# Performance work log

Hardware: AMD Instinct MI355X
Metric: run time of the kernel (lower is better)

Reference implementation:

```python
import jax, jax.numpy as jnp
import numpy as np

CODEBOOK_SIZE = 32768
EMBED_DIM = 4


def setup_inputs() -> dict:
    key = jax.random.key(0)
    k1, k2 = jax.random.split(key)
    # [batch, temporal, channels, height, width]
    hidden_state = jax.random.normal(k1, (1, 4, EMBED_DIM, 48, 48), dtype=jnp.float32)
    # nn.Embedding weight, init uniform(-1/cb, 1/cb) as in the torch module
    embedding = jax.random.uniform(
        k2, (CODEBOOK_SIZE, EMBED_DIM), dtype=jnp.float32,
        minval=-1.0 / CODEBOOK_SIZE, maxval=1.0 / CODEBOOK_SIZE,
    )
    return {"hidden_state": hidden_state, "embedding": embedding}


def reference(hidden_state, embedding):
    b, t, c, h, w = hidden_state.shape
    # permute channels last, flatten to [N, C]
    x = jnp.transpose(hidden_state, (0, 1, 3, 4, 2)).reshape(-1, c)
    distances = (
        jnp.sum(x * x, axis=1, keepdims=True)
        + jnp.sum(embedding * embedding, axis=1)
        - 2.0 * jnp.einsum("nd,kd->nk", x, embedding)
    )
    min_encoding_indices = jnp.argmin(distances, axis=1)
    return min_encoding_indices.reshape(b, t, h, w)
```

## Files before the change

kernel.cpp:

```cpp
#include <hip/hip_runtime.h>
#include <cfloat>


#define ROWS  12
#define BLOCK 512
#define WAVES (BLOCK / 64)
#define NK    32768
#define EPT   2
#define CHUNK (BLOCK * EPT)

__device__ __forceinline__ float rlf(float v) {
    return __builtin_bit_cast(float,
        __builtin_amdgcn_readfirstlane(__builtin_bit_cast(int, v)));
}

__global__ __launch_bounds__(BLOCK)
__attribute__((amdgpu_waves_per_eu(3, 4)))
void vq_argmin_kernel(const float* __restrict__ hs,
                      const float4* __restrict__ cb,
                      int* __restrict__ out)
{
    __shared__ float sRD[WAVES * ROWS];
    __shared__ int   sRI[WAVES * ROWS];

    const int tid = threadIdx.x;
    const int rowbase = blockIdx.x * ROWS;

    float sx0[ROWS], sx1[ROWS], sx2[ROWS], sx3[ROWS], sq[ROWS];
    float best[ROWS];
    int   bidx[ROWS];

    #pragma unroll
    for (int r = 0; r < ROWS; ++r) {
        int n = rowbase + r;
        int t = n / 2304;
        int rem = n - t * 2304;
        const float* ptr = hs + t * 9216 + rem;
        float a0 = ptr[0], a1 = ptr[2304], a2 = ptr[4608], a3 = ptr[6912];
        float q = __fadd_rn(__fadd_rn(__fadd_rn(__fmul_rn(a0, a0),
                                                __fmul_rn(a1, a1)),
                                      __fmul_rn(a2, a2)),
                            __fmul_rn(a3, a3));
        sx0[r] = rlf(a0); sx1[r] = rlf(a1);
        sx2[r] = rlf(a2); sx3[r] = rlf(a3);
        sq[r]  = rlf(q);
        best[r] = FLT_MAX; bidx[r] = 0;
    }

    float4 bufA[EPT], bufB[EPT];

    auto load_chunk = [&](float4* buf, int tb) {
        #pragma unroll
        for (int j = 0; j < EPT; ++j) buf[j] = cb[tb + tid + j * BLOCK];
    };
    auto compute_chunk = [&](const float4* buf, int tb) {
        #pragma unroll
        for (int j = 0; j < EPT; ++j) {
            float4 e = buf[j];
            float e2 = __fadd_rn(__fadd_rn(__fadd_rn(__fmul_rn(e.x, e.x),
                                                     __fmul_rn(e.y, e.y)),
                                           __fmul_rn(e.z, e.z)),
                                 __fmul_rn(e.w, e.w));
            int m = tb / BLOCK + j;
            #pragma unroll
            for (int r = 0; r < ROWS; ++r) {
                float dot = __fmul_rn(sx0[r], e.x);
                dot = __fmaf_rn(sx1[r], e.y, dot);
                dot = __fmaf_rn(sx2[r], e.z, dot);
                dot = __fmaf_rn(sx3[r], e.w, dot);
                float t1 = __fadd_rn(sq[r], e2);
                float d  = __fmaf_rn(dot, -2.0f, t1);
                if (d < best[r]) { best[r] = d; bidx[r] = m; }
            }
        }
    };

    load_chunk(bufA, 0);
    for (int tb = 0; tb < NK; tb += 2 * CHUNK) {
        load_chunk(bufB, tb + CHUNK);
        compute_chunk(bufA, tb);
        int nb = tb + 2 * CHUNK < NK ? tb + 2 * CHUNK : 0;
        load_chunk(bufA, nb);
        compute_chunk(bufB, tb + CHUNK);
    }

    int kk[ROWS];
    #pragma unroll
    for (int r = 0; r < ROWS; ++r) kk[r] = bidx[r] * BLOCK + tid;

    #pragma unroll
    for (int r = 0; r < ROWS; ++r) {
        float d = best[r]; int i = kk[r];
        #pragma unroll
        for (int off = 32; off >= 1; off >>= 1) {
            float d2 = __shfl_xor(d, off, 64);
            int   i2 = __shfl_xor(i, off, 64);
            if (d2 < d || (d2 == d && i2 < i)) { d = d2; i = i2; }
        }
        best[r] = d; kk[r] = i;
    }

    int wave = tid >> 6;
    if ((tid & 63) == 0) {
        #pragma unroll
        for (int r = 0; r < ROWS; ++r) {
            sRD[wave * ROWS + r] = best[r];
            sRI[wave * ROWS + r] = kk[r];
        }
    }
    __syncthreads();

    if (tid < ROWS) {
        float d = sRD[tid]; int i = sRI[tid];
        #pragma unroll
        for (int w = 1; w < WAVES; ++w) {
            float d2 = sRD[w * ROWS + tid];
            int   i2 = sRI[w * ROWS + tid];
            if (d2 < d || (d2 == d && i2 < i)) { d = d2; i = i2; }
        }
        out[rowbase + tid] = i;
    }
}

extern "C" void kernel_launch(void* const* d_in, const int* in_sizes, int n_in,
                              void* d_out, int out_size, void* d_ws, size_t ws_size,
                              hipStream_t stream)
{
    const float*  hs = (const float*)d_in[0];
    const float4* cb = (const float4*)d_in[1];
    int* out = (int*)d_out;

    const int nrows = 9216;
    dim3 grid(nrows / ROWS), block(BLOCK);
    vq_argmin_kernel<<<grid, block, 0, stream>>>(hs, cb, out);
}
```

Baseline: 121.8 us.

## Split codebook across blocks with per-row atomicMin on packed distance-index keys

```diff
diff --git a/kernel.cpp b/kernel.cpp
--- a/kernel.cpp
+++ b/kernel.cpp
@@ -2,124 +2,91 @@
 #include <cfloat>
 
 
-#define ROWS  12
-#define BLOCK 512
-#define WAVES (BLOCK / 64)
+#define NROWS 9216
 #define NK    32768
-#define EPT   2
-#define CHUNK (BLOCK * EPT)
+#define RGSZ  256
+#define NRG   (NROWS / RGSZ)
+#define SEGS  64
+#define SEGSZ (NK / SEGS)
 
-__device__ __forceinline__ float rlf(float v) {
-    return __builtin_bit_cast(float,
-        __builtin_amdgcn_readfirstlane(__builtin_bit_cast(int, v)));
+__device__ __forceinline__ float sq4(float4 e) {
+    return __fadd_rn(__fadd_rn(__fadd_rn(__fmul_rn(e.x, e.x),
+                                         __fmul_rn(e.y, e.y)),
+                               __fmul_rn(e.z, e.z)),
+                     __fmul_rn(e.w, e.w));
 }
 
-__global__ __launch_bounds__(BLOCK)
-__attribute__((amdgpu_waves_per_eu(3, 4)))
-void vq_argmin_kernel(const float* __restrict__ hs,
-                      const float4* __restrict__ cb,
-                      int* __restrict__ out)
+__global__ __launch_bounds__(256)
+void vq_prep(const float4* __restrict__ cb, float* __restrict__ e2t,
+             unsigned long long* __restrict__ keys)
 {
-    __shared__ float sRD[WAVES * ROWS];
-    __shared__ int   sRI[WAVES * ROWS];
+    int k = blockIdx.x * 256 + threadIdx.x;
+    e2t[k] = sq4(cb[k]);
+    if (k < NROWS) keys[k] = ~0ull;
+}
 
-    const int tid = threadIdx.x;
-    const int rowbase = blockIdx.x * ROWS;
+__global__ __launch_bounds__(256)
+void vq_main(const float* __restrict__ hs, const float4* __restrict__ cb,
+             const float* __restrict__ e2t, unsigned long long* __restrict__ keys)
+{
+    const int rg  = blockIdx.x % NRG;
+    const int seg = blockIdx.x / NRG;
 
-    float sx0[ROWS], sx1[ROWS], sx2[ROWS], sx3[ROWS], sq[ROWS];
-    float best[ROWS];
-    int   bidx[ROWS];
+    const int n   = rg * RGSZ + threadIdx.x;
+    const int t   = n / 2304;
+    const int rem = n - t * 2304;
+    const float* p = hs + t * 9216 + rem;
+    const float x0 = p[0], x1 = p[2304], x2 = p[4608], x3 = p[6912];
+    const float xq = __fadd_rn(__fadd_rn(__fadd_rn(__fmul_rn(x0, x0),
+                                                   __fmul_rn(x1, x1)),
+                                         __fmul_rn(x2, x2)),
+                               __fmul_rn(x3, x3));
 
-    #pragma unroll
-    for (int r = 0; r < ROWS; ++r) {
-        int n = rowbase + r;
-        int t = n / 2304;
-        int rem = n - t * 2304;
-        const float* ptr = hs + t * 9216 + rem;
-        float a0 = ptr[0], a1 = ptr[2304], a2 = ptr[4608], a3 = ptr[6912];
-        float q = __fadd_rn(__fadd_rn(__fadd_rn(__fmul_rn(a0, a0),
-                                                __fmul_rn(a1, a1)),
-                                      __fmul_rn(a2, a2)),
-                            __fmul_rn(a3, a3));
-        sx0[r] = rlf(a0); sx1[r] = rlf(a1);
-        sx2[r] = rlf(a2); sx3[r] = rlf(a3);
-        sq[r]  = rlf(q);
-        best[r] = FLT_MAX; bidx[r] = 0;
-    }
+    const int base = seg * SEGSZ;
+    float best = FLT_MAX;
+    int   bk   = 0;
 
-    float4 bufA[EPT], bufB[EPT];
+    float4 eA[4], eB[4];
+    float  qA[4], qB[4];
 
-    auto load_chunk = [&](float4* buf, int tb) {
+    auto ldg = [&](float4* e, float* q, int jj) {
+        int o = (base + jj) & (NK - 1);
         #pragma unroll
-        for (int j = 0; j < EPT; ++j) buf[j] = cb[tb + tid + j * BLOCK];
+        for (int u = 0; u < 4; ++u) { e[u] = cb[o + u]; q[u] = e2t[o + u]; }
     };
-    auto compute_chunk = [&](const float4* buf, int tb) {
+    auto comp = [&](const float4* e, const float* q, int j0) {
         #pragma unroll
-        for (int j = 0; j < EPT; ++j) {
-            float4 e = buf[j];
-            float e2 = __fadd_rn(__fadd_rn(__fadd_rn(__fmul_rn(e.x, e.x),
-                                                     __fmul_rn(e.y, e.y)),
-                                           __fmul_rn(e.z, e.z)),
-                                 __fmul_rn(e.w, e.w));
-            int m = tb / BLOCK + j;
-            #pragma unroll
-            for (int r = 0; r < ROWS; ++r) {
-                float dot = __fmul_rn(sx0[r], e.x);
-                dot = __fmaf_rn(sx1[r], e.y, dot);
-                dot = __fmaf_rn(sx2[r], e.z, dot);
-                dot = __fmaf_rn(sx3[r], e.w, dot);
-                float t1 = __fadd_rn(sq[r], e2);
-                float d  = __fmaf_rn(dot, -2.0f, t1);
-                if (d < best[r]) { best[r] = d; bidx[r] = m; }
-            }
+        for (int u = 0; u < 4; ++u) {
+            float dot = __fmul_rn(x0, e[u].x);
+            dot = __fmaf_rn(x1, e[u].y, dot);
+            dot = __fmaf_rn(x2, e[u].z, dot);
+            dot = __fmaf_rn(x3, e[u].w, dot);
+            float t1 = __fadd_rn(xq, q[u]);
+            float d  = __fmaf_rn(dot, -2.0f, t1);
+            if (d < best) { best = d; bk = base + j0 + u; }
         }
     };
 
-    load_chunk(bufA, 0);
-    for (int tb = 0; tb < NK; tb += 2 * CHUNK) {
-        load_chunk(bufB, tb + CHUNK);
-        compute_chunk(bufA, tb);
-        int nb = tb + 2 * CHUNK < NK ? tb + 2 * CHUNK : 0;
-        load_chunk(bufA, nb);
-        compute_chunk(bufB, tb + CHUNK);
+    ldg(eA, qA, 0);
+    for (int j = 0; j < SEGSZ; j += 8) {
+        ldg(eB, qB, j + 4);
+        comp(eA, qA, j);
+        ldg(eA, qA, j + 8);
+        comp(eB, qB, j + 4);
     }
 
-    int kk[ROWS];
-    #pragma unroll
-    for (int r = 0; r < ROWS; ++r) kk[r] = bidx[r] * BLOCK + tid;
+    unsigned long long key =
+        ((unsigned long long)__builtin_bit_cast(unsigned, best) << 32) |
+        (unsigned)bk;
+    atomicMin(keys + n, key);
+}
 
-    #pragma unroll
-    for (int r = 0; r < ROWS; ++r) {
-        float d = best[r]; int i = kk[r];
-        #pragma unroll
-        for (int off = 32; off >= 1; off >>= 1) {
-            float d2 = __shfl_xor(d, off, 64);
-            int   i2 = __shfl_xor(i, off, 64);
-            if (d2 < d || (d2 == d && i2 < i)) { d = d2; i = i2; }
-        }
-        best[r] = d; kk[r] = i;
-    }
-
-    int wave = tid >> 6;
-    if ((tid & 63) == 0) {
-        #pragma unroll
-        for (int r = 0; r < ROWS; ++r) {
-            sRD[wave * ROWS + r] = best[r];
-            sRI[wave * ROWS + r] = kk[r];
-        }
-    }
-    __syncthreads();
-
-    if (tid < ROWS) {
-        float d = sRD[tid]; int i = sRI[tid];
-        #pragma unroll
-        for (int w = 1; w < WAVES; ++w) {
-            float d2 = sRD[w * ROWS + tid];
-            int   i2 = sRI[w * ROWS + tid];
-            if (d2 < d || (d2 == d && i2 < i)) { d = d2; i = i2; }
-        }
-        out[rowbase + tid] = i;
-    }
+__global__ __launch_bounds__(256)
+void vq_extract(const unsigned long long* __restrict__ keys,
+                int* __restrict__ out)
+{
+    int n = blockIdx.x * 256 + threadIdx.x;
+    out[n] = (int)(keys[n] & 0xFFFFFFFFull);
 }
 
 extern "C" void kernel_launch(void* const* d_in, const int* in_sizes, int n_in,
@@ -130,7 +97,10 @@
     const float4* cb = (const float4*)d_in[1];
     int* out = (int*)d_out;
 
-    const int nrows = 9216;
-    dim3 grid(nrows / ROWS), block(BLOCK);
-    vq_argmin_kernel<<<grid, block, 0, stream>>>(hs, cb, out);
+    unsigned long long* keys = (unsigned long long*)d_ws;
+    float* e2t = (float*)((char*)d_ws + NROWS * sizeof(unsigned long long));
+
+    vq_prep<<<NK / 256, 256, 0, stream>>>(cb, e2t, keys);
+    vq_main<<<NRG * SEGS, 256, 0, stream>>>(hs, cb, e2t, keys);
+    vq_extract<<<NROWS / 256, 256, 0, stream>>>(keys, out);
 }
```

After: 145.9 us. +19.8%, slower.

## Precompute codebook norms in prep kernel and merge two-candidate argmin updates

Applied to the files above, without the earlier changes.

```diff
diff --git a/kernel.cpp b/kernel.cpp
--- a/kernel.cpp
+++ b/kernel.cpp
@@ -5,6 +5,7 @@
 #define ROWS  12
 #define BLOCK 512
 #define WAVES (BLOCK / 64)
+#define NROWS 9216
 #define NK    32768
 #define EPT   2
 #define CHUNK (BLOCK * EPT)
@@ -14,10 +15,22 @@
         __builtin_amdgcn_readfirstlane(__builtin_bit_cast(int, v)));
 }
 
+__global__ __launch_bounds__(256)
+void vq_prep(const float4* __restrict__ cb, float* __restrict__ e2t)
+{
+    int k = blockIdx.x * 256 + threadIdx.x;
+    float4 e = cb[k];
+    e2t[k] = __fadd_rn(__fadd_rn(__fadd_rn(__fmul_rn(e.x, e.x),
+                                           __fmul_rn(e.y, e.y)),
+                                 __fmul_rn(e.z, e.z)),
+                       __fmul_rn(e.w, e.w));
+}
+
 __global__ __launch_bounds__(BLOCK)
 __attribute__((amdgpu_waves_per_eu(3, 4)))
 void vq_argmin_kernel(const float* __restrict__ hs,
                       const float4* __restrict__ cb,
+                      const float* __restrict__ e2t,
                       int* __restrict__ out)
 {
     __shared__ float sRD[WAVES * ROWS];
@@ -47,41 +60,51 @@
         best[r] = FLT_MAX; bidx[r] = 0;
     }
 
-    float4 bufA[EPT], bufB[EPT];
+    float4 eA[EPT], eB[EPT];
+    float  qA[EPT], qB[EPT];
 
-    auto load_chunk = [&](float4* buf, int tb) {
-        #pragma unroll
-        for (int j = 0; j < EPT; ++j) buf[j] = cb[tb + tid + j * BLOCK];
-    };
-    auto compute_chunk = [&](const float4* buf, int tb) {
+    auto load_chunk = [&](float4* e, float* q, int tb) {
         #pragma unroll
         for (int j = 0; j < EPT; ++j) {
-            float4 e = buf[j];
-            float e2 = __fadd_rn(__fadd_rn(__fadd_rn(__fmul_rn(e.x, e.x),
-                                                     __fmul_rn(e.y, e.y)),
-                                           __fmul_rn(e.z, e.z)),
-                                 __fmul_rn(e.w, e.w));
-            int m = tb / BLOCK + j;
-            #pragma unroll
-            for (int r = 0; r < ROWS; ++r) {
-                float dot = __fmul_rn(sx0[r], e.x);
-                dot = __fmaf_rn(sx1[r], e.y, dot);
-                dot = __fmaf_rn(sx2[r], e.z, dot);
-                dot = __fmaf_rn(sx3[r], e.w, dot);
-                float t1 = __fadd_rn(sq[r], e2);
-                float d  = __fmaf_rn(dot, -2.0f, t1);
-                if (d < best[r]) { best[r] = d; bidx[r] = m; }
-            }
+            e[j] = cb[tb + tid + j * BLOCK];
+            q[j] = e2t[tb + tid + j * BLOCK];
+        }
+    };
+    auto compute_chunk = [&](const float4* e, const float* q, int tb) {
+        float4 ea = e[0], eb = e[1];
+        float  qa = q[0], qb = q[1];
+        int m1 = tb / BLOCK;
+        int m2 = m1 + 1;
+        #pragma unroll
+        for (int r = 0; r < ROWS; ++r) {
+            float dota = __fmul_rn(sx0[r], ea.x);
+            dota = __fmaf_rn(sx1[r], ea.y, dota);
+            dota = __fmaf_rn(sx2[r], ea.z, dota);
+            dota = __fmaf_rn(sx3[r], ea.w, dota);
+            float ta = __fadd_rn(sq[r], qa);
+            float da = __fmaf_rn(dota, -2.0f, ta);
+
+            float dotb = __fmul_rn(sx0[r], eb.x);
+            dotb = __fmaf_rn(sx1[r], eb.y, dotb);
+            dotb = __fmaf_rn(sx2[r], eb.z, dotb);
+            dotb = __fmaf_rn(sx3[r], eb.w, dotb);
+            float tb2 = __fadd_rn(sq[r], qb);
+            float db = __fmaf_rn(dotb, -2.0f, tb2);
+
+            float nb = fminf(fminf(best[r], da), db);
+            int   w  = (da <= db) ? m1 : m2;
+            if (nb < best[r]) bidx[r] = w;
+            best[r] = nb;
         }
     };
 
-    load_chunk(bufA, 0);
+    load_chunk(eA, qA, 0);
     for (int tb = 0; tb < NK; tb += 2 * CHUNK) {
-        load_chunk(bufB, tb + CHUNK);
-        compute_chunk(bufA, tb);
-        int nb = tb + 2 * CHUNK < NK ? tb + 2 * CHUNK : 0;
-        load_chunk(bufA, nb);
-        compute_chunk(bufB, tb + CHUNK);
+        load_chunk(eB, qB, tb + CHUNK);
+        compute_chunk(eA, qA, tb);
+        int nb2 = tb + 2 * CHUNK < NK ? tb + 2 * CHUNK : 0;
+        load_chunk(eA, qA, nb2);
+        compute_chunk(eB, qB, tb + CHUNK);
     }
 
     int kk[ROWS];
@@ -130,7 +153,10 @@
     const float4* cb = (const float4*)d_in[1];
     int* out = (int*)d_out;
 
-    const int nrows = 9216;
-    dim3 grid(nrows / ROWS), block(BLOCK);
-    vq_argmin_kernel<<<grid, block, 0, stream>>>(hs, cb, out);
+    float* e2t = (float*)d_ws;
+
+    vq_prep<<<NK / 256, 256, 0, stream>>>(cb, e2t);
+
+    dim3 grid(NROWS / ROWS), block(BLOCK);
+    vq_argmin_kernel<<<grid, block, 0, stream>>>(hs, cb, e2t, out);
 }
```

New measurement: 119.5 us. About the same (-1.9%).
